# Performance work log

Hardware: AMD Instinct MI355X
Metric: run time of the kernel (lower is better)

## Reference

```python
import jax, jax.numpy as jnp
import numpy as np

N = 50000      # n_nodes
E = 800000     # edges (before self-loops)
IN = 128       # in_dim
HID = 32       # hidden_dim (per-head out channels)
HEADS = 4
EMB = 128      # embed_dim
LAYERS = 3
NEG_SLOPE = 0.2  # PyG GATv2 default leaky_relu slope


def _layer_norm(x, g, b):
    mu = jnp.mean(x, axis=-1, keepdims=True)
    var = jnp.var(x, axis=-1, keepdims=True)
    return g * (x - mu) / jnp.sqrt(var + 1e-5) + b


def _gatv2(h, src, dst, n, Wl, bl, Wr, br, att, bias):
    # GATv2Conv (PyG semantics, share_weights=False, concat=True).
    H, C = att.shape
    xl = (h @ Wl + bl).reshape(n, H, C)   # target (i) transform
    xr = (h @ Wr + br).reshape(n, H, C)   # source (j) transform
    x_i = xl[dst]                          # [Etot, H, C] gather
    x_j = xr[src]
    e = jax.nn.leaky_relu(x_i + x_j, NEG_SLOPE)
    logit = jnp.einsum('ehc,hc->eh', e, att)          # [Etot, H]
    # segment softmax over destination node (every node has a self-loop)
    m = jax.ops.segment_max(logit, dst, num_segments=n)
    ex = jnp.exp(logit - m[dst])
    den = jax.ops.segment_sum(ex, dst, num_segments=n)
    alpha = ex / (den[dst] + 1e-16)
    out = jax.ops.segment_sum(alpha[..., None] * x_j, dst, num_segments=n)
    return out.reshape(n, H * C) + bias


def setup_inputs() -> dict:
    key = jax.random.key(0)
    ks = iter(jax.random.split(key, 64))
    d = {}
    d['x'] = jax.random.normal(next(ks), (N, IN), jnp.float32)
    d['edge_index'] = jax.random.randint(next(ks), (2, E), 0, N, dtype=jnp.int64)

    def w(shape, fan):
        return jax.random.normal(next(ks), shape, jnp.float32) / np.float32(np.sqrt(fan))

    HC = HID * HEADS
    d['W_in'] = w((IN, HID), IN); d['b_in'] = jnp.zeros((HID,), jnp.float32)
    for i in range(LAYERS):
        ic = HID if i == 0 else HC
        d[f'Wl{i}'] = w((ic, HC), ic); d[f'bl{i}'] = jnp.zeros((HC,), jnp.float32)
        d[f'Wr{i}'] = w((ic, HC), ic); d[f'br{i}'] = jnp.zeros((HC,), jnp.float32)
        d[f'att{i}'] = w((HEADS, HID), HID)
        d[f'bo{i}'] = jnp.zeros((HC,), jnp.float32)
        d[f'g{i}'] = jnp.ones((HC,), jnp.float32)
        d[f'be{i}'] = jnp.zeros((HC,), jnp.float32)
    d['W_out'] = w((HC, EMB), HC); d['b_out'] = jnp.zeros((EMB,), jnp.float32)
    return d


def reference(x, edge_index, W_in, b_in,
              Wl0, bl0, Wr0, br0, att0, bo0, g0, be0,
              Wl1, bl1, Wr1, br1, att1, bo1, g1, be1,
              Wl2, bl2, Wr2, br2, att2, bo2, g2, be2,
              W_out, b_out):
    n = x.shape[0]
    loops = jnp.arange(n, dtype=edge_index.dtype)  # add_self_loops=True
    src = jnp.concatenate([edge_index[0], loops])
    dst = jnp.concatenate([edge_index[1], loops])

    h = jax.nn.gelu(x @ W_in + b_in, approximate=False)
    layers = [(Wl0, bl0, Wr0, br0, att0, bo0, g0, be0),
              (Wl1, bl1, Wr1, br1, att1, bo1, g1, be1),
              (Wl2, bl2, Wr2, br2, att2, bo2, g2, be2)]
    for (Wl, bl, Wr, br, att, bo, g, be) in layers:
        h_new = jax.nn.gelu(_layer_norm(_gatv2(h, src, dst, n, Wl, bl, Wr, br, att, bo), g, be), approximate=False)
        h = h + h_new if h.shape == h_new.shape else h_new  # dropout = identity (eval)
    out = h @ W_out + b_out
    norm = jnp.maximum(jnp.linalg.norm(out, axis=-1, keepdims=True), 1e-12)
    return out / norm
```

## Files before the change

### kernel.cpp

```cpp
#include <hip/hip_runtime.h>
#include <hip/hip_bf16.h>
#include <math.h>

#define N_NODES 50000
#define N_EDGES 800000
#define IN_DIM  128
#define HC_DIM  128
#define HID_C   32
#define SCAN_NB 196
#define LOG2E   1.4426950408889634f

typedef __attribute__((ext_vector_type(8))) short short8;
typedef __attribute__((ext_vector_type(4))) short short4v;
typedef __attribute__((ext_vector_type(4))) float f32x4;

__device__ __forceinline__ float gelu_f(float x){
    return 0.5f*x*(1.0f + erff(x*0.7071067811865475f));
}

__device__ __forceinline__ void split2(float f, short& h, short& l){
    __hip_bfloat16 bh = __float2bfloat16(f);
    float r = f - __bfloat162float(bh);
    __hip_bfloat16 blo = __float2bfloat16(r);
    h = *reinterpret_cast<short*>(&bh);
    l = *reinterpret_cast<short*>(&blo);
}
__device__ __forceinline__ unsigned short f2bf(float f){
    __hip_bfloat16 b = __float2bfloat16(f);
    return *reinterpret_cast<unsigned short*>(&b);
}
__device__ __forceinline__ float bf2f(unsigned short u){
    return __uint_as_float(((unsigned)u)<<16);
}

__global__ __launch_bounds__(256) void k_count(const int* __restrict__ dst, int* __restrict__ cnt,
                                               int* __restrict__ rank){
    int b = blockIdx.x*1024 + threadIdx.x;
    #pragma unroll
    for(int i=0;i<4;i++){
        int e = b + i*256;
        if(e < N_EDGES) rank[e] = atomicAdd(&cnt[dst[e]], 1);
    }
}

__global__ __launch_bounds__(256) void k_scan1(const int* __restrict__ cnt, int* __restrict__ rowptr,
                                               int* __restrict__ part){
    __shared__ int sh[256];
    int t=threadIdx.x; int i=blockIdx.x*256+t;
    int v = (i<N_NODES)? cnt[i] : 0;
    sh[t]=v; __syncthreads();
    for(int off=1; off<256; off<<=1){
        int y = (t>=off)? sh[t-off] : 0;
        __syncthreads();
        sh[t] += y;
        __syncthreads();
    }
    if(i<N_NODES) rowptr[i] = sh[t]-v;
    if(t==255) part[blockIdx.x] = sh[255];
}

__global__ __launch_bounds__(256) void k_scan2(int* __restrict__ part){
    __shared__ int sh[256];
    int t=threadIdx.x;
    int v = (t<SCAN_NB)? part[t] : 0;
    sh[t]=v; __syncthreads();
    for(int off=1; off<256; off<<=1){
        int y=(t>=off)? sh[t-off]:0;
        __syncthreads();
        sh[t]+=y;
        __syncthreads();
    }
    if(t<SCAN_NB) part[t] = sh[t]-v;
}

__global__ __launch_bounds__(256) void k_scan3(int* __restrict__ rowptr, const int* __restrict__ part){
    int t=threadIdx.x; int i=blockIdx.x*256+t;
    if(i<N_NODES) rowptr[i] += part[blockIdx.x];
    if(i==0) rowptr[N_NODES]=N_EDGES;
}

__global__ __launch_bounds__(256) void k_fill(const int* __restrict__ src, const int* __restrict__ dst,
                                              const int* __restrict__ rowptr, const int* __restrict__ rank,
                                              int* __restrict__ col){
    int b = blockIdx.x*1024 + threadIdx.x;
    #pragma unroll
    for(int i=0;i<4;i++){
        int e = b + i*256;
        if(e < N_EDGES) col[rowptr[dst[e]] + rank[e]] = src[e];
    }
}

__global__ __launch_bounds__(256) void k_splitW(const float* __restrict__ W0, const float* __restrict__ W1,
                                                const float* __restrict__ W2, const float* __restrict__ W3,
                                                const float* __restrict__ W4, const float* __restrict__ W5,
                                                const float* __restrict__ W6, short* __restrict__ WT){
    int bx = blockIdx.x;
    int m, kc;
    if(bx < 2){ m = bx; kc = 0; }
    else { m = 2 + (bx-2)/4; kc = (bx-2)&3; }
    const float* src; int K; size_t off;
    switch(m){
        case 0: src=W0; K=32;  off=0;      break;
        case 1: src=W1; K=32;  off=8192;   break;
        case 2: src=W2; K=128; off=16384;  break;
        case 3: src=W3; K=128; off=49152;  break;
        case 4: src=W4; K=128; off=81920;  break;
        case 5: src=W5; K=128; off=114688; break;
        default:src=W6; K=128; off=147456; break;
    }
    short* hi = WT + off;
    short* lo = hi + (size_t)K*HC_DIM;
    #pragma unroll
    for(int i=0;i<16;i++){
        int idx = threadIdx.x + i*256;
        int k = kc*32 + (idx>>7);
        int n = idx & 127;
        float f = src[(size_t)k*HC_DIM + n];
        short h,l; split2(f,h,l);
        hi[(size_t)n*K + k] = h;
        lo[(size_t)n*K + k] = l;
    }
}

__global__ __launch_bounds__(256) void k_gemm_in(const float* __restrict__ x, const float* __restrict__ W,
                                                 const float* __restrict__ b, float* __restrict__ h,
                                                 short* __restrict__ hhi, short* __restrict__ hlo){
    int id = blockIdx.x*256+threadIdx.x;
    int r = id>>5, c = id&31;
    const float4* x4 = (const float4*)(x + (size_t)r*IN_DIM);
    float acc=0.f;
    #pragma unroll 8
    for(int k=0;k<IN_DIM/4;k++){
        float4 xv = x4[k];
        acc = fmaf(xv.x, W[(4*k  )*HID_C+c], acc);
        acc = fmaf(xv.y, W[(4*k+1)*HID_C+c], acc);
        acc = fmaf(xv.z, W[(4*k+2)*HID_C+c], acc);
        acc = fmaf(xv.w, W[(4*k+3)*HID_C+c], acc);
    }
    float v = gelu_f(acc + b[c]);
    h[(size_t)r*HID_C+c] = v;
    short hh,ll; split2(v,hh,ll);
    hhi[(size_t)r*HID_C+c] = hh;
    hlo[(size_t)r*HID_C+c] = ll;
}

template<int K, bool PAIR, bool NORM>
__global__ __launch_bounds__(256) void k_mfma(const short* __restrict__ Ahi, const short* __restrict__ Alo,
                                              const short* __restrict__ WTl, const float* __restrict__ bl,
                                              const short* __restrict__ WTr, const float* __restrict__ br,
                                              float* __restrict__ XL, unsigned short* __restrict__ XR16){
    constexpr int LDS_K = 40;
    constexpr int NCH = K / 32;
    __shared__ short As_hi[64*LDS_K], As_lo[64*LDS_K];
    __shared__ short Bh0[128*LDS_K], Bl0[128*LDS_K];
    __shared__ short Bh1[PAIR?128*LDS_K:1], Bl1[PAIR?128*LDS_K:1];
    __shared__ float ssq[NORM?256:1];

    int t = threadIdx.x;
    int lane = t & 63, wave = t >> 6;
    int quad = lane >> 4, ml = lane & 15;
    int rbase = blockIdx.x * 64;

    const short* WTl_lo = WTl + (size_t)K*HC_DIM;
    const short* WTr_lo = PAIR ? (WTr + (size_t)K*HC_DIM) : nullptr;

    f32x4 accL[4][2], accR[4][2];
    #pragma unroll
    for(int i=0;i<4;i++)
        #pragma unroll
        for(int j=0;j<2;j++){ accL[i][j]=(f32x4){0,0,0,0}; accR[i][j]=(f32x4){0,0,0,0}; }

    int r = t >> 2, seg = t & 3;
    int gr = rbase + r; if(gr >= N_NODES) gr = N_NODES-1;

    for(int c=0; c<NCH; c++){
        if(c) __syncthreads();
        size_t ka = (size_t)gr*K + c*32 + seg*8;
        *(short8*)(As_hi + r*LDS_K + seg*8) = *(const short8*)(Ahi + ka);
        *(short8*)(As_lo + r*LDS_K + seg*8) = *(const short8*)(Alo + ka);
        #pragma unroll
        for(int u=0; u<2; u++){
            int uu = t + u*256;
            int n = uu >> 2, sg = uu & 3;
            size_t kw = (size_t)n*K + c*32 + sg*8;
            *(short8*)(Bh0 + n*LDS_K + sg*8) = *(const short8*)(WTl + kw);
            *(short8*)(Bl0 + n*LDS_K + sg*8) = *(const short8*)(WTl_lo + kw);
            if(PAIR){
                *(short8*)(Bh1 + n*LDS_K + sg*8) = *(const short8*)(WTr + kw);
                *(short8*)(Bl1 + n*LDS_K + sg*8) = *(const short8*)(WTr_lo + kw);
            }
        }
        __syncthreads();

        int k0 = quad*8;
        short8 ah[4], al[4];
        #pragma unroll
        for(int i=0;i<4;i++){
            ah[i] = *(const short8*)(As_hi + (16*i + ml)*LDS_K + k0);
            al[i] = *(const short8*)(As_lo + (16*i + ml)*LDS_K + k0);
        }
        #pragma unroll
        for(int j=0;j<2;j++){
            int nrow = j*64 + wave*16 + ml;
            short8 bh = *(const short8*)(Bh0 + nrow*LDS_K + k0);
            short8 blo = *(const short8*)(Bl0 + nrow*LDS_K + k0);
            #pragma unroll
            for(int i=0;i<4;i++){
                accL[i][j] = __builtin_amdgcn_mfma_f32_16x16x32_bf16(ah[i], bh,  accL[i][j], 0,0,0);
                accL[i][j] = __builtin_amdgcn_mfma_f32_16x16x32_bf16(ah[i], blo, accL[i][j], 0,0,0);
                accL[i][j] = __builtin_amdgcn_mfma_f32_16x16x32_bf16(al[i], bh,  accL[i][j], 0,0,0);
            }
            if(PAIR){
                short8 ch = *(const short8*)(Bh1 + nrow*LDS_K + k0);
                short8 cl = *(const short8*)(Bl1 + nrow*LDS_K + k0);
                #pragma unroll
                for(int i=0;i<4;i++){
                    accR[i][j] = __builtin_amdgcn_mfma_f32_16x16x32_bf16(ah[i], ch, accR[i][j], 0,0,0);
                    accR[i][j] = __builtin_amdgcn_mfma_f32_16x16x32_bf16(ah[i], cl, accR[i][j], 0,0,0);
                    accR[i][j] = __builtin_amdgcn_mfma_f32_16x16x32_bf16(al[i], ch, accR[i][j], 0,0,0);
                }
            }
        }
    }

    int col0 = wave*16 + ml, col1 = 64 + wave*16 + ml;
    float bL0 = bl[col0], bL1 = bl[col1];

    if(NORM){
        #pragma unroll
        for(int i=0;i<4;i++){
            #pragma unroll
            for(int rr=0;rr<4;rr++){
                float v0 = accL[i][0][rr] + bL0;
                float v1 = accL[i][1][rr] + bL1;
                float p = v0*v0 + v1*v1;
                p += __shfl_xor(p,1); p += __shfl_xor(p,2);
                p += __shfl_xor(p,4); p += __shfl_xor(p,8);
                if(ml==0) ssq[wave*64 + 16*i + quad*4 + rr] = p;
            }
        }
        __syncthreads();
        #pragma unroll
        for(int i=0;i<4;i++){
            #pragma unroll
            for(int rr=0;rr<4;rr++){
                int row = 16*i + quad*4 + rr;
                int grr = rbase + row;
                if(grr < N_NODES){
                    float tot = ssq[row] + ssq[64+row] + ssq[128+row] + ssq[192+row];
                    float inv = 1.0f / fmaxf(sqrtf(tot), 1e-12f);
                    XL[(size_t)grr*HC_DIM + col0] = (accL[i][0][rr] + bL0) * inv;
                    XL[(size_t)grr*HC_DIM + col1] = (accL[i][1][rr] + bL1) * inv;
                }
            }
        }
    } else {
        float bR0 = PAIR ? br[col0] : 0.f, bR1 = PAIR ? br[col1] : 0.f;
        #pragma unroll
        for(int i=0;i<4;i++){
            #pragma unroll
            for(int rr=0;rr<4;rr++){
                int grr = rbase + 16*i + quad*4 + rr;
                if(grr < N_NODES){
                    XL[(size_t)grr*HC_DIM + col0] = accL[i][0][rr] + bL0;
                    XL[(size_t)grr*HC_DIM + col1] = accL[i][1][rr] + bL1;
                    if(PAIR){
                        XR16[(size_t)grr*HC_DIM + col0] = f2bf(accR[i][0][rr] + bR0);
                        XR16[(size_t)grr*HC_DIM + col1] = f2bf(accR[i][1][rr] + bR1);
                    }
                }
            }
        }
    }
}

__global__ __launch_bounds__(256) void k_node(const float* __restrict__ XL, const unsigned short* __restrict__ XR,
    const int* __restrict__ rowptr, const int* __restrict__ colidx,
    const float* __restrict__ att, const float* __restrict__ bo,
    const float* __restrict__ gg, const float* __restrict__ be,
    const float* __restrict__ hold, float* __restrict__ hout,
    short* __restrict__ hi_out, short* __restrict__ lo_out)
{
    int wave=threadIdx.x>>6, lane=threadIdx.x&63;
    int node = blockIdx.x*4+wave;
    int cg = lane & 31, half = lane >> 5;
    int c4 = cg << 2;

    float4 xl = *(const float4*)(XL + (size_t)node*HC_DIM + c4);
    float4 av = *(const float4*)(att + c4);
    av.x *= LOG2E; av.y *= LOG2E; av.z *= LOG2E; av.w *= LOG2E;
    int beg = rowptr[node], end = rowptr[node+1];

    #define LOADX(j, xx) { ushort4 u_ = *(const ushort4*)(XR + (size_t)(j)*HC_DIM + c4); \
        xx = make_float4(bf2f(u_.x), bf2f(u_.y), bf2f(u_.z), bf2f(u_.w)); }
    #define EDGE_LOGIT(xj, q) { \
        float u0 = xl.x + xj.x; u0 = fmaxf(u0, 0.2f*u0); \
        float u1 = xl.y + xj.y; u1 = fmaxf(u1, 0.2f*u1); \
        float u2 = xl.z + xj.z; u2 = fmaxf(u2, 0.2f*u2); \
        float u3 = xl.w + xj.w; u3 = fmaxf(u3, 0.2f*u3); \
        q = fmaf(u0,av.x, fmaf(u1,av.y, fmaf(u2,av.z, u3*av.w))); \
        q += __shfl_xor(q,1); q += __shfl_xor(q,2); q += __shfl_xor(q,4); }

    float4 xs; LOADX(node, xs)
    float qs; EDGE_LOGIT(xs, qs)
    float m, ls; float4 acc;
    if(half==0){ m = qs; ls = 1.f; acc = xs; }
    else       { m = -INFINITY; ls = 0.f; acc = make_float4(0.f,0.f,0.f,0.f); }

    int P = end - beg;
    int nb = P >> 3;
    int base = beg;
    for(int b=0; b<nb; b++, base += 8){
        int j0 = colidx[base     + half];
        int j1 = colidx[base + 2 + half];
        int j2 = colidx[base + 4 + half];
        int j3 = colidx[base + 6 + half];
        float4 x0, x1, x2, x3;
        LOADX(j0, x0) LOADX(j1, x1) LOADX(j2, x2) LOADX(j3, x3)
        float q0,q1,q2,q3;
        EDGE_LOGIT(x0,q0) EDGE_LOGIT(x1,q1) EDGE_LOGIT(x2,q2) EDGE_LOGIT(x3,q3)
        float nm = fmaxf(m, fmaxf(fmaxf(q0,q1),fmaxf(q2,q3)));
        float sc = exp2f(m-nm);
        float e0 = exp2f(q0-nm), e1 = exp2f(q1-nm);
        float e2 = exp2f(q2-nm), e3 = exp2f(q3-nm);
        ls = fmaf(ls, sc, (e0+e1)+(e2+e3));
        acc.x = fmaf(acc.x, sc, fmaf(e0,x0.x, fmaf(e1,x1.x, fmaf(e2,x2.x, e3*x3.x))));
        acc.y = fmaf(acc.y, sc, fmaf(e0,x0.y, fmaf(e1,x1.y, fmaf(e2,x2.y, e3*x3.y))));
        acc.z = fmaf(acc.z, sc, fmaf(e0,x0.z, fmaf(e1,x1.z, fmaf(e2,x2.z, e3*x3.z))));
        acc.w = fmaf(acc.w, sc, fmaf(e0,x0.w, fmaf(e1,x1.w, fmaf(e2,x2.w, e3*x3.w))));
        m = nm;
    }
    if(base < end){
        int i0 = base + half, i1 = base + 2 + half, i2 = base + 4 + half, i3 = base + 6 + half;
        int j0 = (i0<end)? colidx[i0] : node;
        int j1 = (i1<end)? colidx[i1] : node;
        int j2 = (i2<end)? colidx[i2] : node;
        int j3 = (i3<end)? colidx[i3] : node;
        float4 x0, x1, x2, x3;
        LOADX(j0, x0) LOADX(j1, x1) LOADX(j2, x2) LOADX(j3, x3)
        float q0,q1,q2,q3;
        EDGE_LOGIT(x0,q0) EDGE_LOGIT(x1,q1) EDGE_LOGIT(x2,q2) EDGE_LOGIT(x3,q3)
        if(i1>=end) q1 = -INFINITY;
        if(i2>=end) q2 = -INFINITY;
        if(i3>=end) q3 = -INFINITY;
        if(i0 < end){
            float nm = fmaxf(m, fmaxf(fmaxf(q0,q1),fmaxf(q2,q3)));
            float sc = exp2f(m-nm);
            float e0 = exp2f(q0-nm), e1 = exp2f(q1-nm);
            float e2 = exp2f(q2-nm), e3 = exp2f(q3-nm);
            ls = fmaf(ls, sc, (e0+e1)+(e2+e3));
            acc.x = fmaf(acc.x, sc, fmaf(e0,x0.x, fmaf(e1,x1.x, fmaf(e2,x2.x, e3*x3.x))));
            acc.y = fmaf(acc.y, sc, fmaf(e0,x0.y, fmaf(e1,x1.y, fmaf(e2,x2.y, e3*x3.y))));
            acc.z = fmaf(acc.z, sc, fmaf(e0,x0.z, fmaf(e1,x1.z, fmaf(e2,x2.z, e3*x3.z))));
            acc.w = fmaf(acc.w, sc, fmaf(e0,x0.w, fmaf(e1,x1.w, fmaf(e2,x2.w, e3*x3.w))));
            m = nm;
        }
    }
    #undef EDGE_LOGIT
    #undef LOADX

    {
        float mo  = __shfl_xor(m, 32);
        float lso = __shfl_xor(ls, 32);
        float4 ao;
        ao.x = __shfl_xor(acc.x,32); ao.y = __shfl_xor(acc.y,32);
        ao.z = __shfl_xor(acc.z,32); ao.w = __shfl_xor(acc.w,32);
        float nm = fmaxf(m, mo);
        float s0 = exp2f(m-nm), s1 = exp2f(mo-nm);
        ls = ls*s0 + lso*s1;
        acc.x = acc.x*s0 + ao.x*s1;
        acc.y = acc.y*s0 + ao.y*s1;
        acc.z = acc.z*s0 + ao.z*s1;
        acc.w = acc.w*s0 + ao.w*s1;
    }

    float inv = 1.0f/ls;
    float4 bo4 = *(const float4*)(bo + c4);
    float o0 = fmaf(acc.x,inv,bo4.x), o1 = fmaf(acc.y,inv,bo4.y);
    float o2 = fmaf(acc.z,inv,bo4.z), o3 = fmaf(acc.w,inv,bo4.w);
    float s1v = (o0+o1)+(o2+o3);
    float s2v = fmaf(o0,o0, fmaf(o1,o1, fmaf(o2,o2, o3*o3)));
    #pragma unroll
    for(int msk=1;msk<32;msk<<=1){ s1v += __shfl_xor(s1v,msk); s2v += __shfl_xor(s2v,msk); }
    float mean = s1v*(1.f/128.f);
    float var  = s2v*(1.f/128.f) - mean*mean;
    float rstd = rsqrtf(var + 1e-5f);
    float4 g4  = *(const float4*)(gg + c4);
    float4 be4 = *(const float4*)(be + c4);
    float r0 = gelu_f(fmaf(g4.x*(o0-mean), rstd, be4.x));
    float r1 = gelu_f(fmaf(g4.y*(o1-mean), rstd, be4.y));
    float r2 = gelu_f(fmaf(g4.z*(o2-mean), rstd, be4.z));
    float r3 = gelu_f(fmaf(g4.w*(o3-mean), rstd, be4.w));
    if(hold){
        float4 hv = *(const float4*)(hold + (size_t)node*HC_DIM + c4);
        r0 += hv.x; r1 += hv.y; r2 += hv.z; r3 += hv.w;
    }
    if(half==0){
        *(float4*)(hout + (size_t)node*HC_DIM + c4) = make_float4(r0,r1,r2,r3);
        short4v vh, vl; short hh, ll;
        split2(r0,hh,ll); vh[0]=hh; vl[0]=ll;
        split2(r1,hh,ll); vh[1]=hh; vl[1]=ll;
        split2(r2,hh,ll); vh[2]=hh; vl[2]=ll;
        split2(r3,hh,ll); vh[3]=hh; vl[3]=ll;
        *(short4v*)(hi_out + (size_t)node*HC_DIM + c4) = vh;
        *(short4v*)(lo_out + (size_t)node*HC_DIM + c4) = vl;
    }
}

extern "C" void kernel_launch(void* const* d_in, const int* in_sizes, int n_in,
                              void* d_out, int out_size, void* d_ws, size_t ws_size,
                              hipStream_t stream)
{
    const float* x   = (const float*)d_in[0];
    const int*   ei  = (const int*)  d_in[1];
    const float* Win = (const float*)d_in[2];
    const float* bin = (const float*)d_in[3];
    const float *Wl[3], *bl[3], *Wr[3], *br[3], *att[3], *bo[3], *gg[3], *be[3];
    for(int i=0;i<3;i++){
        const int base = 4 + 8*i;
        Wl[i]=(const float*)d_in[base+0]; bl[i]=(const float*)d_in[base+1];
        Wr[i]=(const float*)d_in[base+2]; br[i]=(const float*)d_in[base+3];
        att[i]=(const float*)d_in[base+4]; bo[i]=(const float*)d_in[base+5];
        gg[i]=(const float*)d_in[base+6]; be[i]=(const float*)d_in[base+7];
    }
    const float* Wout=(const float*)d_in[28];
    const float* bout=(const float*)d_in[29];
    float* out = (float*)d_out;

    char* w = (char*)d_ws;
    float* hA = (float*)w;  w += (size_t)N_NODES*HC_DIM*4;
    float* hB = (float*)w;  w += (size_t)N_NODES*HC_DIM*4;
    float* XL = (float*)w;  w += (size_t)N_NODES*HC_DIM*4;
    unsigned short* XR16 = (unsigned short*)w; w += (size_t)N_NODES*HC_DIM*2;
    short* hAhi = (short*)w; w += (size_t)N_NODES*HC_DIM*2;
    short* hAlo = (short*)w; w += (size_t)N_NODES*HC_DIM*2;
    short* hBhi = (short*)w; w += (size_t)N_NODES*HC_DIM*2;
    short* hBlo = (short*)w; w += (size_t)N_NODES*HC_DIM*2;
    short* WT   = (short*)w; w += (size_t)180224*2;
    int* rowptr = (int*)w;  w += (size_t)(N_NODES+2)*4;
    int* cursor = (int*)w;  w += (size_t)N_NODES*4;
    int* colidx = (int*)w;  w += (size_t)N_EDGES*4;
    int* rank   = (int*)w;  w += (size_t)N_EDGES*4;
    int* part   = (int*)w;  w += 256*4;

    const int* srcp = ei;
    const int* dstp = ei + N_EDGES;

    const short* WTl0 = WT + 0;      const short* WTr0 = WT + 8192;
    const short* WTl1 = WT + 16384;  const short* WTr1 = WT + 49152;
    const short* WTl2 = WT + 81920;  const short* WTr2 = WT + 114688;
    const short* WTo  = WT + 147456;

    k_splitW<<<22,256,0,stream>>>(Wl[0],Wr[0],Wl[1],Wr[1],Wl[2],Wr[2],Wout, WT);
    hipMemsetAsync(cursor, 0, (size_t)N_NODES*4, stream);
    k_count <<<782,256, 0, stream>>>(dstp, cursor, rank);
    k_scan1 <<<SCAN_NB,256,0,stream>>>(cursor, rowptr, part);
    k_scan2 <<<1,   256, 0, stream>>>(part);
    k_scan3 <<<SCAN_NB,256,0,stream>>>(rowptr, part);
    k_fill  <<<782,256, 0, stream>>>(srcp, dstp, rowptr, rank, colidx);
    k_gemm_in<<<6250,256,0,stream>>>(x, Win, bin, hA, hAhi, hAlo);

    k_mfma<32,true,false><<<782,256,0,stream>>>(hAhi, hAlo, WTl0, bl[0], WTr0, br[0], XL, XR16);
    k_node<<<12500,256,0,stream>>>(XL,XR16,rowptr,colidx,att[0],bo[0],gg[0],be[0],
                                   (const float*)nullptr, hB, hBhi, hBlo);

    k_mfma<128,true,false><<<782,256,0,stream>>>(hBhi, hBlo, WTl1, bl[1], WTr1, br[1], XL, XR16);
    k_node<<<12500,256,0,stream>>>(XL,XR16,rowptr,colidx,att[1],bo[1],gg[1],be[1], hB, hA, hAhi, hAlo);

    k_mfma<128,true,false><<<782,256,0,stream>>>(hAhi, hAlo, WTl2, bl[2], WTr2, br[2], XL, XR16);
    k_node<<<12500,256,0,stream>>>(XL,XR16,rowptr,colidx,att[2],bo[2],gg[2],be[2], hA, hB, hBhi, hBlo);

    k_mfma<128,false,true><<<782,256,0,stream>>>(hBhi, hBlo, WTo, bout, nullptr, nullptr, out, nullptr);
}
```

Before: 498.1 us.

## Store source features as fp16 and compute edge logits with packed fp16 dot products

The source-transformed features move from bf16 to fp16 storage. The per-node aggregation kernel is restructured so each lane handles 8 channels and a wave processes four edge groups of 4 edges at once, 16 edges per iteration. Edge logits are computed with fdot2 on packed halves, and leaky_relu is rewritten as 0.6*u + 0.4*|u|. This aims to cut VALU work and shuffles per edge and to widen gathers to 16 bytes. In exchange it uses fp16 arithmetic for the logits, which reduces precision, and adds an extra reduction stage across the four groups.

```diff
diff --git a/kernel.cpp b/kernel.cpp
--- a/kernel.cpp
+++ b/kernel.cpp
@@ -13,6 +13,9 @@
 typedef __attribute__((ext_vector_type(8))) short short8;
 typedef __attribute__((ext_vector_type(4))) short short4v;
 typedef __attribute__((ext_vector_type(4))) float f32x4;
+typedef _Float16 hf8 __attribute__((ext_vector_type(8)));
+typedef _Float16 hf2 __attribute__((ext_vector_type(2)));
+typedef unsigned int uint4v __attribute__((ext_vector_type(4)));
 
 __device__ __forceinline__ float gelu_f(float x){
     return 0.5f*x*(1.0f + erff(x*0.7071067811865475f));
@@ -25,12 +28,9 @@
     h = *reinterpret_cast<short*>(&bh);
     l = *reinterpret_cast<short*>(&blo);
 }
-__device__ __forceinline__ unsigned short f2bf(float f){
-    __hip_bfloat16 b = __float2bfloat16(f);
-    return *reinterpret_cast<unsigned short*>(&b);
-}
-__device__ __forceinline__ float bf2f(unsigned short u){
-    return __uint_as_float(((unsigned)u)<<16);
+__device__ __forceinline__ unsigned short f2h(float f){
+    _Float16 h = (_Float16)f;
+    return __builtin_bit_cast(unsigned short, h);
 }
 
 __global__ __launch_bounds__(256) void k_count(const int* __restrict__ dst, int* __restrict__ cnt,
@@ -265,8 +265,8 @@
                     XL[(size_t)grr*HC_DIM + col0] = accL[i][0][rr] + bL0;
                     XL[(size_t)grr*HC_DIM + col1] = accL[i][1][rr] + bL1;
                     if(PAIR){
-                        XR16[(size_t)grr*HC_DIM + col0] = f2bf(accR[i][0][rr] + bR0);
-                        XR16[(size_t)grr*HC_DIM + col1] = f2bf(accR[i][1][rr] + bR1);
+                        XR16[(size_t)grr*HC_DIM + col0] = f2h(accR[i][0][rr] + bR0);
+                        XR16[(size_t)grr*HC_DIM + col1] = f2h(accR[i][1][rr] + bR1);
                     }
                 }
             }
@@ -283,128 +283,158 @@
 {
     int wave=threadIdx.x>>6, lane=threadIdx.x&63;
     int node = blockIdx.x*4+wave;
-    int cg = lane & 31, half = lane >> 5;
-    int c4 = cg << 2;
-
-    float4 xl = *(const float4*)(XL + (size_t)node*HC_DIM + c4);
-    float4 av = *(const float4*)(att + c4);
-    av.x *= LOG2E; av.y *= LOG2E; av.z *= LOG2E; av.w *= LOG2E;
+    int qd = lane >> 4, cl = lane & 15;
+    int c8 = cl << 3;
+
+    const float* xlp = XL + (size_t)node*HC_DIM + c8;
+    float4 xa = *(const float4*)xlp;
+    float4 xb = *(const float4*)(xlp+4);
+    float xlf[8] = {xa.x,xa.y,xa.z,xa.w,xb.x,xb.y,xb.z,xb.w};
+    float4 aa = *(const float4*)(att + c8);
+    float4 abv = *(const float4*)(att + c8 + 4);
+    float af[8] = {aa.x,aa.y,aa.z,aa.w,abv.x,abv.y,abv.z,abv.w};
+    hf8 xlh, av6, av4;
+    const float s6 = 0.6f*LOG2E, s4 = 0.4f*LOG2E;
+    #pragma unroll
+    for(int k=0;k<8;k++){
+        xlh[k] = (_Float16)xlf[k];
+        av6[k] = (_Float16)(af[k]*s6);
+        av4[k] = (_Float16)(af[k]*s4);
+    }
+
     int beg = rowptr[node], end = rowptr[node+1];
 
-    #define LOADX(j, xx) { ushort4 u_ = *(const ushort4*)(XR + (size_t)(j)*HC_DIM + c4); \
-        xx = make_float4(bf2f(u_.x), bf2f(u_.y), bf2f(u_.z), bf2f(u_.w)); }
-    #define EDGE_LOGIT(xj, q) { \
-        float u0 = xl.x + xj.x; u0 = fmaxf(u0, 0.2f*u0); \
-        float u1 = xl.y + xj.y; u1 = fmaxf(u1, 0.2f*u1); \
-        float u2 = xl.z + xj.z; u2 = fmaxf(u2, 0.2f*u2); \
-        float u3 = xl.w + xj.w; u3 = fmaxf(u3, 0.2f*u3); \
-        q = fmaf(u0,av.x, fmaf(u1,av.y, fmaf(u2,av.z, u3*av.w))); \
-        q += __shfl_xor(q,1); q += __shfl_xor(q,2); q += __shfl_xor(q,4); }
-
-    float4 xs; LOADX(node, xs)
-    float qs; EDGE_LOGIT(xs, qs)
-    float m, ls; float4 acc;
-    if(half==0){ m = qs; ls = 1.f; acc = xs; }
-    else       { m = -INFINITY; ls = 0.f; acc = make_float4(0.f,0.f,0.f,0.f); }
+    #define H2(v,k) __builtin_shufflevector(v, v, 2*(k), 2*(k)+1)
+    #define LOADH(j, xv) { xv = *(const hf8*)((const _Float16*)XR + ((size_t)((unsigned)(j)<<7)) + c8); }
+#if defined(__has_builtin) && __has_builtin(__builtin_amdgcn_fdot2)
+    #define LOGIT(xv, q) { \
+        hf8 u_ = xlh + xv; \
+        hf8 a_ = __builtin_bit_cast(hf8, __builtin_bit_cast(uint4v, u_) & 0x7fff7fffu); \
+        float qa_ = __builtin_amdgcn_fdot2(H2(u_,0), H2(av6,0), 0.f, false); \
+        float qb_ = __builtin_amdgcn_fdot2(H2(a_,0), H2(av4,0), 0.f, false); \
+        qa_ = __builtin_amdgcn_fdot2(H2(u_,1), H2(av6,1), qa_, false); \
+        qb_ = __builtin_amdgcn_fdot2(H2(a_,1), H2(av4,1), qb_, false); \
+        qa_ = __builtin_amdgcn_fdot2(H2(u_,2), H2(av6,2), qa_, false); \
+        qb_ = __builtin_amdgcn_fdot2(H2(a_,2), H2(av4,2), qb_, false); \
+        qa_ = __builtin_amdgcn_fdot2(H2(u_,3), H2(av6,3), qa_, false); \
+        qb_ = __builtin_amdgcn_fdot2(H2(a_,3), H2(av4,3), qb_, false); \
+        q = qa_ + qb_; \
+        q += __shfl_xor(q,1); q += __shfl_xor(q,2); }
+#else
+    #define LOGIT(xv, q) { \
+        hf8 u_ = xlh + xv; \
+        hf8 a_ = __builtin_bit_cast(hf8, __builtin_bit_cast(uint4v, u_) & 0x7fff7fffu); \
+        q = 0.f; \
+        _Pragma("unroll") \
+        for(int k_=0;k_<8;k_++) q = fmaf((float)u_[k_], (float)av6[k_], fmaf((float)a_[k_], (float)av4[k_], q)); \
+        q += __shfl_xor(q,1); q += __shfl_xor(q,2); }
+#endif
+    #define UPDATE4 { \
+        float nm = fmaxf(m, fmaxf(fmaxf(q0,q1),fmaxf(q2,q3))); \
+        float sc = exp2f(m-nm); \
+        float e0=exp2f(q0-nm), e1=exp2f(q1-nm), e2=exp2f(q2-nm), e3=exp2f(q3-nm); \
+        ls = fmaf(ls, sc, (e0+e1)+(e2+e3)); \
+        _Pragma("unroll") \
+        for(int k=0;k<8;k++) \
+            acc[k] = fmaf(acc[k], sc, fmaf(e0,(float)x0[k], fmaf(e1,(float)x1[k], fmaf(e2,(float)x2[k], e3*(float)x3[k])))); \
+        m = nm; }
+
+    hf8 xs; LOADH(node, xs)
+    float qs; LOGIT(xs, qs)
+    float m, ls, acc[8];
+    if(qd==0){
+        m = qs; ls = 1.f;
+        #pragma unroll
+        for(int k=0;k<8;k++) acc[k] = (float)xs[k];
+    } else {
+        m = -1e30f; ls = 0.f;
+        #pragma unroll
+        for(int k=0;k<8;k++) acc[k] = 0.f;
+    }
 
     int P = end - beg;
-    int nb = P >> 3;
+    int nb = P >> 4;
     int base = beg;
-    for(int b=0; b<nb; b++, base += 8){
-        int j0 = colidx[base     + half];
-        int j1 = colidx[base + 2 + half];
-        int j2 = colidx[base + 4 + half];
-        int j3 = colidx[base + 6 + half];
-        float4 x0, x1, x2, x3;
-        LOADX(j0, x0) LOADX(j1, x1) LOADX(j2, x2) LOADX(j3, x3)
+    int qoff = qd << 2;
+    for(int b=0; b<nb; b++, base += 16){
+        int b2 = base + qoff;
+        int j0 = colidx[b2], j1 = colidx[b2+1], j2 = colidx[b2+2], j3 = colidx[b2+3];
+        hf8 x0,x1,x2,x3;
+        LOADH(j0,x0) LOADH(j1,x1) LOADH(j2,x2) LOADH(j3,x3)
         float q0,q1,q2,q3;
-        EDGE_LOGIT(x0,q0) EDGE_LOGIT(x1,q1) EDGE_LOGIT(x2,q2) EDGE_LOGIT(x3,q3)
-        float nm = fmaxf(m, fmaxf(fmaxf(q0,q1),fmaxf(q2,q3)));
-        float sc = exp2f(m-nm);
-        float e0 = exp2f(q0-nm), e1 = exp2f(q1-nm);
-        float e2 = exp2f(q2-nm), e3 = exp2f(q3-nm);
-        ls = fmaf(ls, sc, (e0+e1)+(e2+e3));
-        acc.x = fmaf(acc.x, sc, fmaf(e0,x0.x, fmaf(e1,x1.x, fmaf(e2,x2.x, e3*x3.x))));
-        acc.y = fmaf(acc.y, sc, fmaf(e0,x0.y, fmaf(e1,x1.y, fmaf(e2,x2.y, e3*x3.y))));
-        acc.z = fmaf(acc.z, sc, fmaf(e0,x0.z, fmaf(e1,x1.z, fmaf(e2,x2.z, e3*x3.z))));
-        acc.w = fmaf(acc.w, sc, fmaf(e0,x0.w, fmaf(e1,x1.w, fmaf(e2,x2.w, e3*x3.w))));
-        m = nm;
+        LOGIT(x0,q0) LOGIT(x1,q1) LOGIT(x2,q2) LOGIT(x3,q3)
+        UPDATE4
     }
     if(base < end){
-        int i0 = base + half, i1 = base + 2 + half, i2 = base + 4 + half, i3 = base + 6 + half;
-        int j0 = (i0<end)? colidx[i0] : node;
-        int j1 = (i1<end)? colidx[i1] : node;
-        int j2 = (i2<end)? colidx[i2] : node;
-        int j3 = (i3<end)? colidx[i3] : node;
-        float4 x0, x1, x2, x3;
-        LOADX(j0, x0) LOADX(j1, x1) LOADX(j2, x2) LOADX(j3, x3)
+        int b2 = base + qoff;
+        int j0 = (b2  <end)? colidx[b2]   : node;
+        int j1 = (b2+1<end)? colidx[b2+1] : node;
+        int j2 = (b2+2<end)? colidx[b2+2] : node;
+        int j3 = (b2+3<end)? colidx[b2+3] : node;
+        hf8 x0,x1,x2,x3;
+        LOADH(j0,x0) LOADH(j1,x1) LOADH(j2,x2) LOADH(j3,x3)
         float q0,q1,q2,q3;
-        EDGE_LOGIT(x0,q0) EDGE_LOGIT(x1,q1) EDGE_LOGIT(x2,q2) EDGE_LOGIT(x3,q3)
-        if(i1>=end) q1 = -INFINITY;
-        if(i2>=end) q2 = -INFINITY;
-        if(i3>=end) q3 = -INFINITY;
-        if(i0 < end){
-            float nm = fmaxf(m, fmaxf(fmaxf(q0,q1),fmaxf(q2,q3)));
-            float sc = exp2f(m-nm);
-            float e0 = exp2f(q0-nm), e1 = exp2f(q1-nm);
-            float e2 = exp2f(q2-nm), e3 = exp2f(q3-nm);
-            ls = fmaf(ls, sc, (e0+e1)+(e2+e3));
-            acc.x = fmaf(acc.x, sc, fmaf(e0,x0.x, fmaf(e1,x1.x, fmaf(e2,x2.x, e3*x3.x))));
-            acc.y = fmaf(acc.y, sc, fmaf(e0,x0.y, fmaf(e1,x1.y, fmaf(e2,x2.y, e3*x3.y))));
-            acc.z = fmaf(acc.z, sc, fmaf(e0,x0.z, fmaf(e1,x1.z, fmaf(e2,x2.z, e3*x3.z))));
-            acc.w = fmaf(acc.w, sc, fmaf(e0,x0.w, fmaf(e1,x1.w, fmaf(e2,x2.w, e3*x3.w))));
-            m = nm;
-        }
-    }
-    #undef EDGE_LOGIT
-    #undef LOADX
-
-    {
-        float mo  = __shfl_xor(m, 32);
-        float lso = __shfl_xor(ls, 32);
-        float4 ao;
-        ao.x = __shfl_xor(acc.x,32); ao.y = __shfl_xor(acc.y,32);
-        ao.z = __shfl_xor(acc.z,32); ao.w = __shfl_xor(acc.w,32);
+        LOGIT(x0,q0) LOGIT(x1,q1) LOGIT(x2,q2) LOGIT(x3,q3)
+        if(b2+1>=end) q1 = -INFINITY;
+        if(b2+2>=end) q2 = -INFINITY;
+        if(b2+3>=end) q3 = -INFINITY;
+        if(b2 < end){
+            UPDATE4
+        }
+    }
+    #undef UPDATE4
+    #undef LOGIT
+    #undef LOADH
+    #undef H2
+
+    #pragma unroll
+    for(int mk=16; mk<=32; mk<<=1){
+        float mo  = __shfl_xor(m, mk);
+        float lso = __shfl_xor(ls, mk);
+        float ao[8];
+        #pragma unroll
+        for(int k=0;k<8;k++) ao[k] = __shfl_xor(acc[k], mk);
         float nm = fmaxf(m, mo);
         float s0 = exp2f(m-nm), s1 = exp2f(mo-nm);
         ls = ls*s0 + lso*s1;
-        acc.x = acc.x*s0 + ao.x*s1;
-        acc.y = acc.y*s0 + ao.y*s1;
-        acc.z = acc.z*s0 + ao.z*s1;
-        acc.w = acc.w*s0 + ao.w*s1;
+        #pragma unroll
+        for(int k=0;k<8;k++) acc[k] = acc[k]*s0 + ao[k]*s1;
+        m = nm;
     }
 
     float inv = 1.0f/ls;
-    float4 bo4 = *(const float4*)(bo + c4);
-    float o0 = fmaf(acc.x,inv,bo4.x), o1 = fmaf(acc.y,inv,bo4.y);
-    float o2 = fmaf(acc.z,inv,bo4.z), o3 = fmaf(acc.w,inv,bo4.w);
-    float s1v = (o0+o1)+(o2+o3);
-    float s2v = fmaf(o0,o0, fmaf(o1,o1, fmaf(o2,o2, o3*o3)));
-    #pragma unroll
-    for(int msk=1;msk<32;msk<<=1){ s1v += __shfl_xor(s1v,msk); s2v += __shfl_xor(s2v,msk); }
+    float4 b0 = *(const float4*)(bo + c8);
+    float4 b1 = *(const float4*)(bo + c8 + 4);
+    float bof[8] = {b0.x,b0.y,b0.z,b0.w,b1.x,b1.y,b1.z,b1.w};
+    float o[8];
+    #pragma unroll
+    for(int k=0;k<8;k++) o[k] = fmaf(acc[k], inv, bof[k]);
+    float s1v = ((o[0]+o[1])+(o[2]+o[3])) + ((o[4]+o[5])+(o[6]+o[7]));
+    float s2v = o[0]*o[0];
+    #pragma unroll
+    for(int k=1;k<8;k++) s2v = fmaf(o[k],o[k],s2v);
+    #pragma unroll
+    for(int mk=1;mk<16;mk<<=1){ s1v += __shfl_xor(s1v,mk); s2v += __shfl_xor(s2v,mk); }
     float mean = s1v*(1.f/128.f);
     float var  = s2v*(1.f/128.f) - mean*mean;
     float rstd = rsqrtf(var + 1e-5f);
-    float4 g4  = *(const float4*)(gg + c4);
-    float4 be4 = *(const float4*)(be + c4);
-    float r0 = gelu_f(fmaf(g4.x*(o0-mean), rstd, be4.x));
-    float r1 = gelu_f(fmaf(g4.y*(o1-mean), rstd, be4.y));
-    float r2 = gelu_f(fmaf(g4.z*(o2-mean), rstd, be4.z));
-    float r3 = gelu_f(fmaf(g4.w*(o3-mean), rstd, be4.w));
+
+    int ch2 = c8 + (qd<<1);
+    float oa = (qd&2) ? ((qd&1)? o[6] : o[4]) : ((qd&1)? o[2] : o[0]);
+    float ob = (qd&2) ? ((qd&1)? o[7] : o[5]) : ((qd&1)? o[3] : o[1]);
+    float2 g2  = *(const float2*)(gg + ch2);
+    float2 be2 = *(const float2*)(be + ch2);
+    float r0 = gelu_f(fmaf(g2.x*(oa-mean), rstd, be2.x));
+    float r1 = gelu_f(fmaf(g2.y*(ob-mean), rstd, be2.y));
     if(hold){
-        float4 hv = *(const float4*)(hold + (size_t)node*HC_DIM + c4);
-        r0 += hv.x; r1 += hv.y; r2 += hv.z; r3 += hv.w;
-    }
-    if(half==0){
-        *(float4*)(hout + (size_t)node*HC_DIM + c4) = make_float4(r0,r1,r2,r3);
-        short4v vh, vl; short hh, ll;
-        split2(r0,hh,ll); vh[0]=hh; vl[0]=ll;
-        split2(r1,hh,ll); vh[1]=hh; vl[1]=ll;
-        split2(r2,hh,ll); vh[2]=hh; vl[2]=ll;
-        split2(r3,hh,ll); vh[3]=hh; vl[3]=ll;
-        *(short4v*)(hi_out + (size_t)node*HC_DIM + c4) = vh;
-        *(short4v*)(lo_out + (size_t)node*HC_DIM + c4) = vl;
-    }
+        float2 hv = *(const float2*)(hold + (size_t)node*HC_DIM + ch2);
+        r0 += hv.x; r1 += hv.y;
+    }
+    *(float2*)(hout + (size_t)node*HC_DIM + ch2) = make_float2(r0,r1);
+    short h0,l0,h1,l1;
+    split2(r0,h0,l0); split2(r1,h1,l1);
+    *(short2*)(hi_out + (size_t)node*HC_DIM + ch2) = make_short2(h0,h1);
+    *(short2*)(lo_out + (size_t)node*HC_DIM + ch2) = make_short2(l0,l1);
 }
 
 extern "C" void kernel_launch(void* const* d_in, const int* in_sizes, int n_in,
```

Result: no change. 496.6 us (-0.3%).
